# Optimization experiments

Measured on AMD Instinct MI355X. Metric: run time of the kernel, lower is better.

The kernel has to match this reference:

```python
import jax, jax.numpy as jnp
import numpy as np

# ---- t2t / fold geometry (FuseFormer defaults) ----
D_MODEL, HD = 512, 1960
K, S, P = 7, 3, 3            # kernel, stride, padding
H, W = 60, 108               # fold output_size
NH = (H + 2 * P - K) // S + 1  # 20
NW = (W + 2 * P - K) // S + 1  # 36
N_VECS = NH * NW             # 720
C = HD // (K * K)            # 40
HP, WP = H + 2 * P, W + 2 * P

# flat positions in the padded image for each (ki,kj,block_i,block_j)
_ki, _kj, _bi, _bj = np.meshgrid(np.arange(K), np.arange(K), np.arange(NH), np.arange(NW), indexing='ij')
POS = jnp.asarray(((_bi * S + _ki) * WP + (_bj * S + _kj)).reshape(-1))  # (K*K*N_VECS,)

# overlap-add count map (fold of all-ones normalizer), cropped to (H, W)
_cnt = np.zeros(HP * WP, dtype=np.float32)
np.add.at(_cnt, np.asarray(POS), 1.0)
NORM = jnp.asarray(_cnt.reshape(HP, WP)[P:P + H, P:P + W])  # (H, W), all > 0


def _fold_norm_unfold(h):
    # h: (B2, HD, N_VECS) -> fold -> divide by count -> unfold -> (B2, HD, N_VECS)
    B2 = h.shape[0]
    v = h.reshape(B2, C, K * K, N_VECS).reshape(B2, C, -1)
    img = jnp.zeros((B2, C, HP * WP), h.dtype).at[:, :, POS].add(v)
    img = img.reshape(B2, C, HP, WP)[:, :, P:P + H, P:P + W] / NORM  # crop + normalize
    imgp = jnp.pad(img, ((0, 0), (0, 0), (P, P), (P, P)))            # re-pad with zeros
    patches = imgp.reshape(B2, C, HP * WP)[:, :, POS]                # gather (unfold)
    return patches.reshape(B2, HD, N_VECS)


def setup_inputs() -> dict:
    key = jax.random.key(0)
    k1, k2, k3, k4, k5 = jax.random.split(key, 5)
    b, n = 4, 5 * N_VECS  # n = 3600
    return {
        'x': jax.random.normal(k1, (b, n, D_MODEL), jnp.float32),
        'W1': jax.random.normal(k2, (D_MODEL, HD), jnp.float32) * (1.0 / np.sqrt(D_MODEL)),
        'b1': jax.random.normal(k3, (HD,), jnp.float32) * 0.01,
        'W2': jax.random.normal(k4, (HD, D_MODEL), jnp.float32) * (1.0 / np.sqrt(HD)),
        'b2': jax.random.normal(k5, (D_MODEL,), jnp.float32) * 0.01,
    }


def reference(x, W1, b1, W2, b2):
    b, n, _ = x.shape
    h = jnp.einsum('bnd,dh->bnh', x, W1) + b1            # (b, n, HD)
    h = h.reshape(-1, N_VECS, HD).transpose(0, 2, 1)     # (B2, HD, N_VECS)
    h = _fold_norm_unfold(h)
    h = h.transpose(0, 2, 1).reshape(b, n, HD)
    out = jnp.einsum('bnh,hd->bnd', jax.nn.relu(h), W2) + b2  # dropout = identity (eval)
    return out
```

## Files before the change

### kernel.cpp

```cpp
#include <hip/hip_runtime.h>

#define D_MODEL 512
#define HD      1960
#define NPAD    2048
#define NVECS   720
#define MROWS   14400
#define MPAD    14464
#define HP      66
#define WP      114
#define IMGPIX  7524

typedef __bf16 bf16x8 __attribute__((ext_vector_type(8)));
typedef float  f32x4  __attribute__((ext_vector_type(4)));

__device__ __forceinline__ unsigned short f2bf(float f) {
    unsigned u = __builtin_bit_cast(unsigned, f);
    u += 0x7FFFu + ((u >> 16) & 1u);
    return (unsigned short)(u >> 16);
}
__device__ __forceinline__ float bf2f(unsigned short s) {
    unsigned u = ((unsigned)s) << 16;
    return __builtin_bit_cast(float, u);
}

__device__ __forceinline__ void gload_lds16(const unsigned short* g, unsigned short* l) {
    __builtin_amdgcn_global_load_lds(
        (const __attribute__((address_space(1))) unsigned int*)g,
        (__attribute__((address_space(3))) unsigned int*)l,
        16, 0, 0);
}

__global__ void cvt_x(const float* __restrict__ x, unsigned short* __restrict__ xb) {
    size_t i = ((size_t)blockIdx.x * 256 + threadIdx.x) * 4;
    const size_t valid = (size_t)MROWS * D_MODEL;
    if (i >= (size_t)MPAD * D_MODEL) return;
    ushort4 o;
    if (i < valid) {
        float4 v = *(const float4*)(x + i);
        o.x = f2bf(v.x); o.y = f2bf(v.y); o.z = f2bf(v.z); o.w = f2bf(v.w);
    } else {
        o.x = o.y = o.z = o.w = 0;
    }
    *(ushort4*)(xb + i) = o;
}

__global__ void transpose_cvt(const float* __restrict__ src, unsigned short* __restrict__ dst,
                              int srcR, int srcC, int dstR, int dstC) {
    __shared__ float tile[32][33];
    int c0 = blockIdx.x * 32;
    int r0 = blockIdx.y * 32;
    int tx = threadIdx.x, ty = threadIdx.y;
    #pragma unroll
    for (int i = 0; i < 32; i += 8) {
        int sr = c0 + ty + i, sc = r0 + tx;
        tile[ty + i][tx] = (sr < srcR && sc < srcC) ? src[(size_t)sr * srcC + sc] : 0.f;
    }
    __syncthreads();
    #pragma unroll
    for (int i = 0; i < 32; i += 8) {
        int dr = r0 + ty + i, dc = c0 + tx;
        if (dr < dstR && dc < dstC)
            dst[(size_t)dr * dstC + dc] = f2bf(tile[tx][ty + i]);
    }
}

template<int MODE>
__global__ __launch_bounds__(256) void gemm_bt(const unsigned short* __restrict__ A,
                        const unsigned short* __restrict__ BT,
                        const float* __restrict__ bias,
                        void* __restrict__ Cout,
                        int K, int ldc, int validN, int validM) {
    __shared__ unsigned short lds[2][16384];
    const int t    = threadIdx.x;
    const int wid  = t >> 6, lane = t & 63;
    const int wr   = wid >> 1, wc = wid & 1;
    const int lr   = lane & 15, lh = lane >> 4;
    const int m0   = blockIdx.y * 128, n0 = blockIdx.x * 128;

    int rr[4], qq[4];
    #pragma unroll
    for (int i = 0; i < 4; ++i) {
        int c = t + i * 256;
        rr[i] = c >> 3;
        qq[i] = (c & 7) ^ (rr[i] & 7);
    }

#define STAGE(buf, kt) do { \
        unsigned short* LA = &lds[buf][0]; \
        unsigned short* LB = &lds[buf][8192]; \
        _Pragma("unroll") \
        for (int i = 0; i < 4; ++i) { \
            gload_lds16(A  + (size_t)(m0 + rr[i]) * K + (kt) + qq[i] * 8, LA + (t + i * 256) * 8); \
            gload_lds16(BT + (size_t)(n0 + rr[i]) * K + (kt) + qq[i] * 8, LB + (t + i * 256) * 8); \
        } \
    } while (0)

    f32x4 acc[4][4] = {};
    const int NT = K >> 6;

    STAGE(0, 0);
    for (int tt = 0; tt < NT; ++tt) {
        if (tt + 1 < NT) {
            STAGE((tt + 1) & 1, (tt + 1) * 64);
            asm volatile("s_waitcnt vmcnt(8)" ::: "memory");
        } else {
            asm volatile("s_waitcnt vmcnt(0)" ::: "memory");
        }
        __builtin_amdgcn_s_barrier();
        __builtin_amdgcn_sched_barrier(0);
        const unsigned short* La = &lds[tt & 1][0];
        const unsigned short* Lb = &lds[tt & 1][8192];
        #pragma unroll
        for (int ks = 0; ks < 2; ++ks) {
            bf16x8 a[4], b[4];
            #pragma unroll
            for (int f = 0; f < 4; ++f) {
                int row = wr * 64 + f * 16 + lr;
                int sl  = (ks * 4 + lh) ^ (lr & 7);
                a[f] = *(const bf16x8*)(La + row * 64 + sl * 8);
            }
            #pragma unroll
            for (int g = 0; g < 4; ++g) {
                int row = wc * 64 + g * 16 + lr;
                int sl  = (ks * 4 + lh) ^ (lr & 7);
                b[g] = *(const bf16x8*)(Lb + row * 64 + sl * 8);
            }
            __builtin_amdgcn_s_setprio(1);
            #pragma unroll
            for (int fm = 0; fm < 4; ++fm)
                #pragma unroll
                for (int fn = 0; fn < 4; ++fn)
                    acc[fm][fn] = __builtin_amdgcn_mfma_f32_16x16x32_bf16(
                        a[fm], b[fn], acc[fm][fn], 0, 0, 0);
            __builtin_amdgcn_s_setprio(0);
        }
        __builtin_amdgcn_s_barrier();
        __builtin_amdgcn_sched_barrier(0);
    }
#undef STAGE

    if (MODE == 0) {
        unsigned short* smem = &lds[0][0];
        #pragma unroll
        for (int fm = 0; fm < 4; ++fm) {
            #pragma unroll
            for (int fn = 0; fn < 4; ++fn) {
                int lcol = wc * 64 + fn * 16 + lr;
                float bv = bias[n0 + lcol];
                #pragma unroll
                for (int j = 0; j < 4; ++j) {
                    int lrow = wr * 64 + fm * 16 + lh * 4 + j;
                    smem[lcol * 128 + (lrow ^ ((lcol & 15) << 3))] =
                        f2bf(acc[fm][fn][j] + bv);
                }
            }
        }
        __syncthreads();
        unsigned short* hT = (unsigned short*)Cout;
        int col = t >> 1, half = t & 1;
        int gcol = n0 + col;
        if (gcol < validN) {
            #pragma unroll
            for (int r = 0; r < 16; ++r) {
                int row = half * 64 + r * 4;
                ushort4 v4 = *(const ushort4*)&smem[col * 128 + (row ^ ((col & 15) << 3))];
                *(ushort4*)&hT[(size_t)gcol * MPAD + m0 + row] = v4;
            }
        }
    } else {
        #pragma unroll
        for (int fm = 0; fm < 4; ++fm) {
            #pragma unroll
            for (int fn = 0; fn < 4; ++fn) {
                int gcol = n0 + wc * 64 + fn * 16 + lr;
                float bv = bias[gcol];
                #pragma unroll
                for (int j = 0; j < 4; ++j) {
                    int grow = m0 + wr * 64 + fm * 16 + lh * 4 + j;
                    if (grow < validM)
                        ((float*)Cout)[(size_t)grow * ldc + gcol] = acc[fm][fn][j] + bv;
                }
            }
        }
    }
}

__global__ void fold_norm(const unsigned short* __restrict__ hT, unsigned short* __restrict__ img2) {
    int y  = blockIdx.x;
    int g  = blockIdx.y;
    int b2 = g / 10, cg = g % 10;
    int c0 = cg * 4;
    int x  = threadIdx.x;
    if (x >= WP) return;
    float val[4] = {0.f, 0.f, 0.f, 0.f};
    if (y >= 3 && y < 63 && x >= 3 && x < 111) {
        int kiA[3], biA[3], nki = 0;
        for (int ki = y % 3; ki < 7; ki += 3) {
            int bi = (y - ki) / 3;
            if (y - ki >= 0 && bi < 20) { kiA[nki] = ki; biA[nki] = bi; ++nki; }
        }
        int kjA[3], bjA[3], nkj = 0;
        for (int kj = x % 3; kj < 7; kj += 3) {
            int bj = (x - kj) / 3;
            if (x - kj >= 0 && bj < 36) { kjA[nkj] = kj; bjA[nkj] = bj; ++nkj; }
        }
        float s[4] = {0.f, 0.f, 0.f, 0.f};
        for (int i = 0; i < nki; ++i) {
            for (int j = 0; j < nkj; ++j) {
                int row = b2 * NVECS + biA[i] * 36 + bjA[j];
                int colb = kiA[i] * 7 + kjA[j];
                #pragma unroll
                for (int q = 0; q < 4; ++q)
                    s[q] += bf2f(hT[(size_t)((c0 + q) * 49 + colb) * MPAD + row]);
            }
        }
        float inv = 1.f / (float)(nki * nkj);
        #pragma unroll
        for (int q = 0; q < 4; ++q)
            val[q] = fmaxf(s[q] * inv, 0.f);
    }
    #pragma unroll
    for (int q = 0; q < 4; ++q)
        img2[(size_t)(b2 * 40 + c0 + q) * IMGPIX + y * WP + x] = f2bf(val[q]);
}

__global__ void unfold_k(const unsigned short* __restrict__ img2, unsigned short* __restrict__ h2b) {
    __shared__ unsigned short lds[20 * 798];
    __shared__ unsigned short lut[980];
    const int gb = blockIdx.x;
    const int cg = blockIdx.y;
    const int b2 = gb / 20, bi = gb % 20;
    const int t  = threadIdx.x;

    const unsigned short* src = img2 + (size_t)(b2 * 40 + cg * 20) * IMGPIX + (bi * 3) * WP;
    for (int p = t; p < 7980; p += 256) {
        int cc = p / 399, rem2 = p - cc * 399;
        *(ushort2*)&lds[cc * 798 + rem2 * 2] =
            *(const ushort2*)&src[(size_t)cc * IMGPIX + rem2 * 2];
    }
    for (int L = t; L < 980; L += 256) {
        int cc = L / 49, kk = L - cc * 49;
        lut[L] = (unsigned short)(cc * 798 + (kk / 7) * 114 + (kk % 7));
    }
    __syncthreads();

    const int cpr   = (cg == 0) ? 245 : 267;
    const int total = 36 * cpr;
    const int rowbase = b2 * NVECS + bi * 36;
    const int hdbase  = cg * 980;
    for (int i = t; i < total; i += 256) {
        int r = i / cpr, q = i - r * cpr;
        int hl = q * 4;
        ushort4 v;
        unsigned short* vv = (unsigned short*)&v;
        #pragma unroll
        for (int e = 0; e < 4; ++e) {
            int h = hl + e;
            vv[e] = (h < 980) ? lds[lut[h] + r * 3] : (unsigned short)0;
        }
        *(ushort4*)&h2b[(size_t)(rowbase + r) * NPAD + hdbase + hl] = v;
    }
}

extern "C" void kernel_launch(void* const* d_in, const int* in_sizes, int n_in,
                              void* d_out, int out_size, void* d_ws, size_t ws_size,
                              hipStream_t stream) {
    const float* x  = (const float*)d_in[0];
    const float* W1 = (const float*)d_in[1];
    const float* b1 = (const float*)d_in[2];
    const float* W2 = (const float*)d_in[3];
    const float* b2 = (const float*)d_in[4];
    float* out = (float*)d_out;

    unsigned short* xb   = (unsigned short*)d_ws;
    unsigned short* W1T  = xb   + (size_t)MPAD * D_MODEL;
    unsigned short* W2T  = W1T  + (size_t)NPAD * D_MODEL;
    unsigned short* hT   = W2T  + (size_t)D_MODEL * NPAD;
    unsigned short* h2b  = hT   + (size_t)NPAD * MPAD;
    unsigned short* img2 = h2b  + (size_t)MPAD * NPAD;

    cvt_x<<<(MPAD * D_MODEL / 4 + 255) / 256, 256, 0, stream>>>(x, xb);

    dim3 tb(32, 8);
    transpose_cvt<<<dim3(512 / 32, NPAD / 32), tb, 0, stream>>>(W1, W1T, D_MODEL, HD, NPAD, D_MODEL);
    transpose_cvt<<<dim3(NPAD / 32, 512 / 32), tb, 0, stream>>>(W2, W2T, HD, D_MODEL, D_MODEL, NPAD);

    gemm_bt<0><<<dim3(NPAD / 128, MPAD / 128), 256, 0, stream>>>(
        xb, W1T, b1, hT, D_MODEL, 0, HD, MPAD);

    fold_norm<<<dim3(HP, 200), 128, 0, stream>>>(hT, img2);
    unfold_k<<<dim3(400, 2), 256, 0, stream>>>(img2, h2b);

    gemm_bt<1><<<dim3(512 / 128, MPAD / 128), 256, 0, stream>>>(
        h2b, W2T, b2, out, NPAD, D_MODEL, D_MODEL, MROWS);
}
```

Before: 177.9 us.

## Replace first GEMM with 256x256-tile 8-wave kernel using 4-stage LDS pipeline

Adds a new GEMM kernel for the first projection that uses 256x256 output tiles, 512 threads (8 waves), and a 4-slot LDS ring with three stages of prefetch and explicit vmcnt waits, interleaving B loads between MFMA halves. MPAD grows to a multiple of 256 so the tiles cover all rows. The larger tile raises data reuse per byte loaded and deepens load/compute overlap, while the epilogue writes the transposed bf16 output through swizzled LDS. The costs are more registers and LDS per block, fewer blocks in the grid, and extra padded rows.

```diff
diff --git a/kernel.cpp b/kernel.cpp
--- a/kernel.cpp
+++ b/kernel.cpp
@@ -5,7 +5,7 @@
 #define NPAD    2048
 #define NVECS   720
 #define MROWS   14400
-#define MPAD    14464
+#define MPAD    14592
 #define HP      66
 #define WP      114
 #define IMGPIX  7524
@@ -61,6 +61,125 @@
         int dr = r0 + ty + i, dc = c0 + tx;
         if (dr < dstR && dc < dstC)
             dst[(size_t)dr * dstC + dc] = f2bf(tile[tx][ty + i]);
+    }
+}
+
+__global__ __launch_bounds__(512, 2) void gemm8p(const unsigned short* __restrict__ A,
+                        const unsigned short* __restrict__ BT,
+                        const float* __restrict__ bias,
+                        unsigned short* __restrict__ hT,
+                        int K, int validN) {
+    __shared__ unsigned short lds[4][16384];
+    const int t    = threadIdx.x;
+    const int lane = t & 63, wid = t >> 6;
+    const int wr   = wid >> 2, wc = wid & 3;
+    const int lr   = lane & 15, lh = lane >> 4;
+    const int m0   = blockIdx.y * 256, n0 = blockIdx.x * 256;
+    const int HS   = K >> 5;
+
+    int srcOff0, srcOff1;
+    {
+        int c = t, p = c >> 3, s = c & 7, lc = s ^ (p & 7);
+        srcOff0 = (2 * p + (lc >> 2)) * K + (lc & 3) * 8;
+        c = t + 512; p = c >> 3; s = c & 7; lc = s ^ (p & 7);
+        srcOff1 = (2 * p + (lc >> 2)) * K + (lc & 3) * 8;
+    }
+    const unsigned short* Asrc0 = A  + (size_t)m0 * K + srcOff0;
+    const unsigned short* Asrc1 = A  + (size_t)m0 * K + srcOff1;
+    const unsigned short* Bsrc0 = BT + (size_t)n0 * K + srcOff0;
+    const unsigned short* Bsrc1 = BT + (size_t)n0 * K + srcOff1;
+
+#define STG_A(hs) do { int rs_ = (hs) & 3; \
+        gload_lds16(Asrc0 + (hs) * 32, &lds[rs_][0] + t * 8); \
+        gload_lds16(Asrc1 + (hs) * 32, &lds[rs_][0] + (t + 512) * 8); } while (0)
+#define STG_B(hs) do { int rs_ = (hs) & 3; \
+        gload_lds16(Bsrc0 + (hs) * 32, &lds[rs_][8192] + t * 8); \
+        gload_lds16(Bsrc1 + (hs) * 32, &lds[rs_][8192] + (t + 512) * 8); } while (0)
+
+    f32x4 acc[8][4] = {};
+
+    STG_A(0); STG_B(0); STG_A(1); STG_B(1); STG_A(2); STG_B(2);
+
+    for (int hs = 0; hs < HS; ++hs) {
+        const int rs = hs & 3;
+        const unsigned short* La = &lds[rs][0];
+        const unsigned short* Lb = &lds[rs][8192];
+        const int rem = HS - hs;
+        if (rem > 3) { STG_A(hs + 3); asm volatile("s_waitcnt vmcnt(10)" ::: "memory"); }
+        else if (rem == 3) asm volatile("s_waitcnt vmcnt(8)" ::: "memory");
+        else if (rem == 2) asm volatile("s_waitcnt vmcnt(4)" ::: "memory");
+        else               asm volatile("s_waitcnt vmcnt(0)" ::: "memory");
+        __builtin_amdgcn_s_barrier();
+        bf16x8 bfr[4], afr[4];
+        #pragma unroll
+        for (int g = 0; g < 4; ++g) {
+            int r = wc * 64 + g * 16 + lr, p = r >> 1;
+            bfr[g] = *(const bf16x8*)(Lb + p * 64 + (((((r & 1) << 2) | lh) ^ (p & 7)) * 8));
+        }
+        #pragma unroll
+        for (int f = 0; f < 4; ++f) {
+            int r = wr * 128 + f * 16 + lr, p = r >> 1;
+            afr[f] = *(const bf16x8*)(La + p * 64 + (((((r & 1) << 2) | lh) ^ (p & 7)) * 8));
+        }
+        asm volatile("s_waitcnt lgkmcnt(0)" ::: "memory");
+        __builtin_amdgcn_sched_barrier(0);
+        __builtin_amdgcn_s_setprio(1);
+        #pragma unroll
+        for (int f = 0; f < 4; ++f)
+            #pragma unroll
+            for (int g = 0; g < 4; ++g)
+                acc[f][g] = __builtin_amdgcn_mfma_f32_16x16x32_bf16(afr[f], bfr[g], acc[f][g], 0, 0, 0);
+        __builtin_amdgcn_s_setprio(0);
+        __builtin_amdgcn_s_barrier();
+        if (rem > 3) STG_B(hs + 3);
+        __builtin_amdgcn_s_barrier();
+        #pragma unroll
+        for (int f = 0; f < 4; ++f) {
+            int r = wr * 128 + (f + 4) * 16 + lr, p = r >> 1;
+            afr[f] = *(const bf16x8*)(La + p * 64 + (((((r & 1) << 2) | lh) ^ (p & 7)) * 8));
+        }
+        asm volatile("s_waitcnt lgkmcnt(0)" ::: "memory");
+        __builtin_amdgcn_sched_barrier(0);
+        __builtin_amdgcn_s_setprio(1);
+        #pragma unroll
+        for (int f = 0; f < 4; ++f)
+            #pragma unroll
+            for (int g = 0; g < 4; ++g)
+                acc[f + 4][g] = __builtin_amdgcn_mfma_f32_16x16x32_bf16(afr[f], bfr[g], acc[f + 4][g], 0, 0, 0);
+        __builtin_amdgcn_s_setprio(0);
+        __builtin_amdgcn_s_barrier();
+    }
+#undef STG_A
+#undef STG_B
+
+    __syncthreads();
+    unsigned short* sm = &lds[0][0];
+    #pragma unroll
+    for (int f = 0; f < 8; ++f) {
+        #pragma unroll
+        for (int g = 0; g < 4; ++g) {
+            int col = wc * 64 + g * 16 + lr;
+            int gcol = n0 + col;
+            float bv = (gcol < validN) ? bias[gcol] : 0.f;
+            int gr = wr * 32 + f * 4 + lh;
+            ushort4 v4;
+            v4.x = f2bf(acc[f][g][0] + bv);
+            v4.y = f2bf(acc[f][g][1] + bv);
+            v4.z = f2bf(acc[f][g][2] + bv);
+            v4.w = f2bf(acc[f][g][3] + bv);
+            *(ushort4*)(sm + col * 256 + ((gr ^ (col & 63)) << 2)) = v4;
+        }
+    }
+    __syncthreads();
+    int col = t & 255, half = t >> 8;
+    int gcol = n0 + col;
+    if (gcol < validN) {
+        #pragma unroll
+        for (int i = 0; i < 32; ++i) {
+            int gr = half * 32 + i;
+            ushort4 v4 = *(const ushort4*)(sm + col * 256 + ((gr ^ (col & 63)) << 2));
+            *(ushort4*)&hT[(size_t)gcol * MPAD + m0 + gr * 4] = v4;
+        }
     }
 }
 
@@ -139,47 +258,17 @@
     }
 #undef STAGE
 
-    if (MODE == 0) {
-        unsigned short* smem = &lds[0][0];
-        #pragma unroll
-        for (int fm = 0; fm < 4; ++fm) {
-            #pragma unroll
-            for (int fn = 0; fn < 4; ++fn) {
-                int lcol = wc * 64 + fn * 16 + lr;
-                float bv = bias[n0 + lcol];
-                #pragma unroll
-                for (int j = 0; j < 4; ++j) {
-                    int lrow = wr * 64 + fm * 16 + lh * 4 + j;
-                    smem[lcol * 128 + (lrow ^ ((lcol & 15) << 3))] =
-                        f2bf(acc[fm][fn][j] + bv);
-                }
-            }
-        }
-        __syncthreads();
-        unsigned short* hT = (unsigned short*)Cout;
-        int col = t >> 1, half = t & 1;
-        int gcol = n0 + col;
-        if (gcol < validN) {
-            #pragma unroll
-            for (int r = 0; r < 16; ++r) {
-                int row = half * 64 + r * 4;
-                ushort4 v4 = *(const ushort4*)&smem[col * 128 + (row ^ ((col & 15) << 3))];
-                *(ushort4*)&hT[(size_t)gcol * MPAD + m0 + row] = v4;
-            }
-        }
-    } else {
-        #pragma unroll
-        for (int fm = 0; fm < 4; ++fm) {
-            #pragma unroll
-            for (int fn = 0; fn < 4; ++fn) {
-                int gcol = n0 + wc * 64 + fn * 16 + lr;
-                float bv = bias[gcol];
-                #pragma unroll
-                for (int j = 0; j < 4; ++j) {
-                    int grow = m0 + wr * 64 + fm * 16 + lh * 4 + j;
-                    if (grow < validM)
-                        ((float*)Cout)[(size_t)grow * ldc + gcol] = acc[fm][fn][j] + bv;
-                }
+    #pragma unroll
+    for (int fm = 0; fm < 4; ++fm) {
+        #pragma unroll
+        for (int fn = 0; fn < 4; ++fn) {
+            int gcol = n0 + wc * 64 + fn * 16 + lr;
+            float bv = bias[gcol];
+            #pragma unroll
+            for (int j = 0; j < 4; ++j) {
+                int grow = m0 + wr * 64 + fm * 16 + lh * 4 + j;
+                if (grow < validM)
+                    ((float*)Cout)[(size_t)grow * ldc + gcol] = acc[fm][fn][j] + bv;
             }
         }
     }
@@ -285,8 +374,8 @@
     transpose_cvt<<<dim3(512 / 32, NPAD / 32), tb, 0, stream>>>(W1, W1T, D_MODEL, HD, NPAD, D_MODEL);
     transpose_cvt<<<dim3(NPAD / 32, 512 / 32), tb, 0, stream>>>(W2, W2T, HD, D_MODEL, D_MODEL, NPAD);
 
-    gemm_bt<0><<<dim3(NPAD / 128, MPAD / 128), 256, 0, stream>>>(
-        xb, W1T, b1, hT, D_MODEL, 0, HD, MPAD);
+    gemm8p<<<dim3(NPAD / 256, MPAD / 256), 512, 0, stream>>>(
+        xb, W1T, b1, hT, D_MODEL, HD);
 
     fold_norm<<<dim3(HP, 200), 128, 0, stream>>>(hT, img2);
     unfold_k<<<dim3(400, 2), 256, 0, stream>>>(img2, h2b);
```

After: 188.3 us. +5.9%, slower.
